# Optimization experiments

Hardware: AMD Instinct MI355X
Metric: run time of the kernel (lower is better)

The kernel has to match this reference:

```python
import jax, jax.numpy as jnp
import numpy as np

NEG = -9e15
ALPHA = 0.2  # leaky-relu slope


def gat_layer(h, mask, W, a, concat):
    # h: [N, Fin], W: [Fin, Fout], a: [2*Fout, 1], mask: [N, N]
    Wh = h @ W                                   # [N, Fout]
    F = Wh.shape[1]
    e = jax.nn.leaky_relu(Wh @ a[:F] + (Wh @ a[F:]).T, ALPHA)  # [N, N]
    att = jax.nn.softmax(jnp.where(mask > 0, e, NEG), axis=1)
    out = att @ Wh                               # [N, Fout]
    return jax.nn.elu(out) if concat else out


def gat(x, mask, W, a, Wo, ao):
    # W: [H, Fin, Fhid], a: [H, 2*Fhid, 1]
    heads = jax.vmap(lambda Wi, ai: gat_layer(x, mask, Wi, ai, True))(W, a)  # [H, N, Fhid]
    h = jnp.transpose(heads, (1, 0, 2)).reshape(x.shape[0], -1)  # [N, H*Fhid] (concat dim=1)
    return jax.nn.elu(gat_layer(h, mask, Wo, ao, False))


def setup_inputs() -> dict:
    key = jax.random.key(0)
    ks = jax.random.split(key, 16)
    N, Fin, H, Fhid, Ffin, P = 4096, 256, 4, 64, 64, 16
    x = jax.random.normal(ks[0], (N, Fin), jnp.float32)
    eye = jnp.eye(N, dtype=jnp.float32)
    sadj = jnp.maximum((jax.random.uniform(ks[1], (N, N)) < 0.005).astype(jnp.float32), eye)
    sadj2 = jnp.maximum((jax.random.uniform(ks[2], (N, N)) < 0.005).astype(jnp.float32), eye)
    s = 0.1
    inp = {
        "x": x, "sadj": sadj, "sadj2": sadj2,
        "W1": s * jax.random.normal(ks[3], (H, Fin, Fhid), jnp.float32),
        "a1": s * jax.random.normal(ks[4], (H, 2 * Fhid, 1), jnp.float32),
        "Wo1": s * jax.random.normal(ks[5], (H * Fhid, Ffin), jnp.float32),
        "ao1": s * jax.random.normal(ks[6], (2 * Ffin, 1), jnp.float32),
        "W2": s * jax.random.normal(ks[7], (H, Fin, Fhid), jnp.float32),
        "a2": s * jax.random.normal(ks[8], (H, 2 * Fhid, 1), jnp.float32),
        "Wo2": s * jax.random.normal(ks[9], (H * Fhid, Ffin), jnp.float32),
        "ao2": s * jax.random.normal(ks[10], (2 * Ffin, 1), jnp.float32),
        "Wp1": s * jax.random.normal(ks[11], (Ffin, P), jnp.float32),
        "bp1": jnp.zeros((P,), jnp.float32),
        "Wp2": s * jax.random.normal(ks[12], (P, 1), jnp.float32),
    }
    return inp


def reference(x, sadj, sadj2, W1, a1, Wo1, ao1, W2, a2, Wo2, ao2, Wp1, bp1, Wp2):
    emb1 = gat(x, sadj, W1, a1, Wo1, ao1)    # [N, Ffin]
    emb2 = gat(x, sadj2, W2, a2, Wo2, ao2)   # [N, Ffin]
    emb = jnp.stack([emb1, emb2], axis=1)    # [N, 2, Ffin]
    w = jnp.tanh(emb @ Wp1 + bp1) @ Wp2      # [N, 2, 1]
    beta = jax.nn.softmax(w, axis=1)
    return jnp.sum(beta * emb, axis=1)       # [N, Ffin]
```

## Files before the change

kernel.cpp:

```cpp
#include <hip/hip_runtime.h>
#include <hip/hip_bf16.h>
#include <stdint.h>


typedef short short8 __attribute__((ext_vector_type(8)));
typedef __bf16 bf16x8 __attribute__((ext_vector_type(8)));
typedef float floatx4 __attribute__((ext_vector_type(4)));

#define MAXDEG 128
#define LRELU 0.2f

template <typename V>
__device__ inline auto mfma_impl(V a, V b, floatx4 c, int)
    -> decltype(__builtin_amdgcn_mfma_f32_16x16x32_bf16(a, b, c, 0, 0, 0)) {
  return __builtin_amdgcn_mfma_f32_16x16x32_bf16(a, b, c, 0, 0, 0);
}
template <typename V>
__device__ inline floatx4 mfma_impl(V a, V b, floatx4 c, long) {
  return __builtin_amdgcn_mfma_f32_16x16x32_bf16(
      __builtin_bit_cast(bf16x8, a), __builtin_bit_cast(bf16x8, b), c, 0, 0, 0);
}
__device__ inline floatx4 MFMA16(short8 a, short8 b, floatx4 c) {
  return mfma_impl(a, b, c, 0);
}

__device__ inline bool is_bf16_inputs(const void* sadj) {
  return ((*(const uint32_t*)sadj) & 0xFFFFu) == 0x3F80u;
}
__device__ inline float ldval(const void* p, size_t i, bool isbf) {
  if (isbf) return __bfloat162float(((const __hip_bfloat16*)p)[i]);
  return ((const float*)p)[i];
}
__device__ inline uint16_t f2bf_bits(float f) {
  __hip_bfloat16 h = __float2bfloat16(f);
  return *(uint16_t*)&h;
}

static constexpr size_t OFF_ADJ = 0;
static constexpr size_t OFF_DEG = OFF_ADJ + (size_t)2 * 4096 * MAXDEG * 4;
static constexpr size_t OFF_XB  = OFF_DEG + (size_t)2 * 4096 * 4;
static constexpr size_t OFF_WT  = OFF_XB  + (size_t)4096 * 256 * 2;
static constexpr size_t OFF_WOT = OFF_WT  + (size_t)2 * 4 * 64 * 256 * 2;
static constexpr size_t OFF_AV  = OFF_WOT + (size_t)2 * 64 * 256 * 2;
static constexpr size_t OFF_AOV = OFF_AV  + (size_t)2 * 4 * 128 * 4;
static constexpr size_t OFF_WP1 = OFF_AOV + (size_t)2 * 128 * 4;
static constexpr size_t OFF_BP1 = OFF_WP1 + (size_t)64 * 16 * 4;
static constexpr size_t OFF_WP2 = OFF_BP1 + 64;
static constexpr size_t OFF_WH1 = OFF_WP2 + 192;
static constexpr size_t OFF_S1  = OFF_WH1 + (size_t)2 * 4096 * 256 * 4;
static constexpr size_t OFF_D1  = OFF_S1  + (size_t)2 * 4 * 4096 * 4;
static constexpr size_t OFF_H2  = OFF_D1  + (size_t)2 * 4 * 4096 * 4;
static constexpr size_t OFF_WH2 = OFF_H2  + (size_t)2 * 4096 * 256 * 2;
static constexpr size_t OFF_S2  = OFF_WH2 + (size_t)2 * 4096 * 64 * 4;
static constexpr size_t OFF_D2  = OFF_S2  + (size_t)2 * 4096 * 4;
static constexpr size_t OFF_EMB = OFF_D2  + (size_t)2 * 4096 * 4;

__global__ __launch_bounds__(256) void k_conv_x(const void* x, const void* sadj,
                                                uint16_t* xb) {
  bool isbf = is_bf16_inputs(sadj);
  int i0 = (blockIdx.x * 256 + threadIdx.x) * 4;
  if (isbf) {
    *(uint64_t*)(xb + i0) = *(const uint64_t*)((const uint16_t*)x + i0);
  } else {
    const float* xf = (const float*)x;
    float4 f = *(const float4*)(xf + i0);
    xb[i0 + 0] = f2bf_bits(f.x);
    xb[i0 + 1] = f2bf_bits(f.y);
    xb[i0 + 2] = f2bf_bits(f.z);
    xb[i0 + 3] = f2bf_bits(f.w);
  }
}

__global__ __launch_bounds__(256) void k_conv_w(const void* W1, const void* W2,
    const void* Wo1, const void* Wo2,
    const void* a1, const void* a2, const void* ao1, const void* ao2,
    const void* wp1, const void* bp1, const void* wp2, const void* sadj,
    uint16_t* Wt, uint16_t* Wot,
    float* Av, float* Aov, float* Wp1v, float* Bp1v, float* Wp2v) {
  bool isbf = is_bf16_inputs(sadj);
  int idx = blockIdx.x * 256 + threadIdx.x;
  if (idx < 131072) {
    int k = idx & 255, f = (idx >> 8) & 63, h = (idx >> 14) & 3, g = idx >> 16;
    const void* W = g ? W2 : W1;
    Wt[idx] = f2bf_bits(ldval(W, (size_t)h * 16384 + (size_t)k * 64 + f, isbf));
  } else if (idx < 163840) {
    int j = idx - 131072;
    int k = j & 255, f = (j >> 8) & 63, g = j >> 14;
    const void* W = g ? Wo2 : Wo1;
    Wot[j] = f2bf_bits(ldval(W, (size_t)k * 64 + f, isbf));
  } else if (idx < 166176) {
    int q = idx - 163840;
    if (q < 512)        Av[q] = ldval(a1, q, isbf);
    else if (q < 1024)  Av[q - 512 + 512] = 0.f, Av[q] = ldval(a2, q - 512, isbf);
    else if (q < 1152)  Aov[q - 1024] = ldval(ao1, q - 1024, isbf);
    else if (q < 1280)  Aov[q - 1152 + 128] = ldval(ao2, q - 1152, isbf);
    else if (q < 2304)  Wp1v[q - 1280] = ldval(wp1, q - 1280, isbf);
    else if (q < 2320)  Bp1v[q - 2304] = ldval(bp1, q - 2304, isbf);
    else                Wp2v[q - 2320] = ldval(wp2, q - 2320, isbf);
  }
}

__global__ __launch_bounds__(256) void k_adj(const void* sadj, const void* sadj2,
                                             int* adj, int* deg) {
  int w = blockIdx.x * 4 + (threadIdx.x >> 6);
  int lane = threadIdx.x & 63;
  int g = w >> 12, n = w & 4095;
  bool isbf = is_bf16_inputs(sadj);
  const void* mask = g ? sadj2 : sadj;
  int* out = adj + (size_t)w * MAXDEG;
  int cnt = 0;
  uint64_t ltmask = (1ull << lane) - 1ull;
  if (isbf) {
    const uint16_t* mrow = (const uint16_t*)mask + (size_t)n * 4096;
    for (int t = 0; t < 8; ++t) {
      int base = t * 512 + lane * 8;
      uint4 v = *(const uint4*)(mrow + base);
      uint32_t words[4] = {v.x, v.y, v.z, v.w};
#pragma unroll
      for (int k = 0; k < 8; ++k) {
        uint16_t val = (uint16_t)(words[k >> 1] >> ((k & 1) * 16));
        bool b = (val != 0) && !(val & 0x8000);
        uint64_t bal = __ballot(b);
        if (b) {
          int pos = cnt + __popcll(bal & ltmask);
          if (pos < MAXDEG) out[pos] = base + k;
        }
        cnt += __popcll(bal);
      }
    }
  } else {
    const float* mrow = (const float*)mask + (size_t)n * 4096;
    for (int t = 0; t < 16; ++t) {
      int base = t * 256 + lane * 4;
      float4 v = *(const float4*)(mrow + base);
      float vals[4] = {v.x, v.y, v.z, v.w};
#pragma unroll
      for (int k = 0; k < 4; ++k) {
        bool b = vals[k] > 0.f;
        uint64_t bal = __ballot(b);
        if (b) {
          int pos = cnt + __popcll(bal & ltmask);
          if (pos < MAXDEG) out[pos] = base + k;
        }
        cnt += __popcll(bal);
      }
    }
  }
  if (lane == 0) deg[w] = cnt < MAXDEG ? cnt : MAXDEG;
}

__global__ __launch_bounds__(256) void k_gemm1(const uint16_t* xb, const uint16_t* Wt,
                                               float* Wh1) {
  int w = blockIdx.x * 4 + (threadIdx.x >> 6);
  int lane = threadIdx.x & 63;
  int q = lane >> 4, c = lane & 15;
  int g = w >> 10, rem = w & 1023;
  int m0 = (rem >> 2) << 4, h = rem & 3;
  const uint16_t* B = Wt + (size_t)(g * 4 + h) * 64 * 256;
  floatx4 acc[4] = {};
  const uint16_t* arow = xb + (size_t)(m0 + c) * 256 + q * 8;
  for (int kk = 0; kk < 8; ++kk) {
    short8 a = *(const short8*)(arow + kk * 32);
#pragma unroll
    for (int t = 0; t < 4; ++t) {
      short8 b = *(const short8*)(B + (size_t)(t * 16 + c) * 256 + kk * 32 + q * 8);
      acc[t] = MFMA16(a, b, acc[t]);
    }
  }
  float* Crow = Wh1 + (size_t)(g * 4096 + m0) * 256 + h * 64;
#pragma unroll
  for (int t = 0; t < 4; ++t)
#pragma unroll
    for (int r = 0; r < 4; ++r)
      Crow[(size_t)(q * 4 + r) * 256 + t * 16 + c] = acc[t][r];
}

__global__ __launch_bounds__(256) void k_gemm2(const uint16_t* h2, const uint16_t* Wot,
                                               float* Wh2) {
  int w = blockIdx.x * 4 + (threadIdx.x >> 6);
  int lane = threadIdx.x & 63;
  int q = lane >> 4, c = lane & 15;
  int g = w >> 8, m0 = (w & 255) << 4;
  const uint16_t* A = h2 + (size_t)g * 4096 * 256;
  const uint16_t* B = Wot + (size_t)g * 64 * 256;
  floatx4 acc[4] = {};
  const uint16_t* arow = A + (size_t)(m0 + c) * 256 + q * 8;
  for (int kk = 0; kk < 8; ++kk) {
    short8 a = *(const short8*)(arow + kk * 32);
#pragma unroll
    for (int t = 0; t < 4; ++t) {
      short8 b = *(const short8*)(B + (size_t)(t * 16 + c) * 256 + kk * 32 + q * 8);
      acc[t] = MFMA16(a, b, acc[t]);
    }
  }
  float* Crow = Wh2 + (size_t)(g * 4096 + m0) * 64;
#pragma unroll
  for (int t = 0; t < 4; ++t)
#pragma unroll
    for (int r = 0; r < 4; ++r)
      Crow[(size_t)(q * 4 + r) * 64 + t * 16 + c] = acc[t][r];
}

__global__ __launch_bounds__(256) void k_sd1(const float* Wh1, const float* Av,
                                             float* s1, float* d1) {
  int w = blockIdx.x * 4 + (threadIdx.x >> 6);
  int lane = threadIdx.x & 63;
  int g = w >> 14, h = (w >> 12) & 3, n = w & 4095;
  float v = Wh1[((size_t)(g * 4096 + n)) * 256 + h * 64 + lane];
  const float* a = Av + (g * 4 + h) * 128;
  float ps = v * a[lane], pd = v * a[64 + lane];
#pragma unroll
  for (int o = 32; o; o >>= 1) {
    ps += __shfl_xor(ps, o);
    pd += __shfl_xor(pd, o);
  }
  if (lane == 0) {
    s1[((size_t)(g * 4096 + n)) * 4 + h] = ps;
    d1[((size_t)(g * 4096 + n)) * 4 + h] = pd;
  }
}

__global__ __launch_bounds__(256) void k_att1(const int* adj, const int* deg,
    const float* s1, const float* d1, const float* Wh1, uint16_t* h2) {
  __shared__ float pbuf[4][4][MAXDEG];
  __shared__ int jbuf[4][MAXDEG];
  int wv = threadIdx.x >> 6, lane = threadIdx.x & 63;
  int w = blockIdx.x * 4 + wv;
  int g = w >> 12;
  int gn = w;
  int dg = deg[gn];
  const int* nbr = adj + (size_t)gn * MAXDEG;
  float4 s4 = *(const float4*)(s1 + (size_t)gn * 4);
  const float4* d4 = (const float4*)(d1) + (size_t)g * 4096;

  bool v0 = lane < dg, v1 = lane + 64 < dg;
  int j0 = 0, j1 = 0;
  if (v0) j0 = nbr[lane];
  if (v1) j1 = nbr[lane + 64];
  float4 dj0 = d4[j0];
  float4 dj1 = d4[j1];
  if (v0) jbuf[wv][lane] = j0;
  if (v1) jbuf[wv][lane + 64] = j1;

  const float ninf = -3.0e38f;
  float sa[4] = {s4.x, s4.y, s4.z, s4.w};
  float d0a[4] = {dj0.x, dj0.y, dj0.z, dj0.w};
  float d1a[4] = {dj1.x, dj1.y, dj1.z, dj1.w};
#pragma unroll
  for (int h = 0; h < 4; ++h) {
    float t0 = sa[h] + d0a[h]; t0 = t0 > 0.f ? t0 : LRELU * t0;
    float t1 = sa[h] + d1a[h]; t1 = t1 > 0.f ? t1 : LRELU * t1;
    float e0 = v0 ? t0 : ninf;
    float e1 = v1 ? t1 : ninf;
    float m = fmaxf(e0, e1);
#pragma unroll
    for (int o = 32; o; o >>= 1) m = fmaxf(m, __shfl_xor(m, o));
    float p0 = v0 ? __expf(e0 - m) : 0.f;
    float p1 = v1 ? __expf(e1 - m) : 0.f;
    float l = p0 + p1;
#pragma unroll
    for (int o = 32; o; o >>= 1) l += __shfl_xor(l, o);
    float inv = __frcp_rn(l);
    pbuf[wv][h][lane] = p0 * inv;
    pbuf[wv][h][lane + 64] = p1 * inv;
  }
  int myh = lane >> 4;
  const float* prow = pbuf[wv][myh];
  const int* jb = jbuf[wv];
  const float4* Wg = (const float4*)(Wh1) + (size_t)g * 4096 * 64;
  float ax = 0.f, ay = 0.f, az = 0.f, aw = 0.f;
  int i = 0;
  for (; i + 4 <= dg; i += 4) {
    int ja = jb[i], jb2 = jb[i + 1], jc = jb[i + 2], jd = jb[i + 3];
    float pa = prow[i], pb = prow[i + 1], pc = prow[i + 2], pd = prow[i + 3];
    float4 wa = Wg[(size_t)ja * 64 + lane];
    float4 wb = Wg[(size_t)jb2 * 64 + lane];
    float4 wc = Wg[(size_t)jc * 64 + lane];
    float4 wd = Wg[(size_t)jd * 64 + lane];
    ax += pa * wa.x + pb * wb.x + pc * wc.x + pd * wd.x;
    ay += pa * wa.y + pb * wb.y + pc * wc.y + pd * wd.y;
    az += pa * wa.z + pb * wb.z + pc * wc.z + pd * wd.z;
    aw += pa * wa.w + pb * wb.w + pc * wc.w + pd * wd.w;
  }
  for (; i < dg; ++i) {
    int j = jb[i];
    float p = prow[i];
    float4 wa = Wg[(size_t)j * 64 + lane];
    ax += p * wa.x; ay += p * wa.y; az += p * wa.z; aw += p * wa.w;
  }
  ax = ax > 0.f ? ax : __expf(ax) - 1.f;
  ay = ay > 0.f ? ay : __expf(ay) - 1.f;
  az = az > 0.f ? az : __expf(az) - 1.f;
  aw = aw > 0.f ? aw : __expf(aw) - 1.f;
  ushort4 o4 = {f2bf_bits(ax), f2bf_bits(ay), f2bf_bits(az), f2bf_bits(aw)};
  *(ushort4*)(h2 + (size_t)gn * 256 + lane * 4) = o4;
}

__global__ __launch_bounds__(256) void k_sd2(const float* Wh2, const float* Aov,
                                             float* s2, float* d2) {
  int w = blockIdx.x * 4 + (threadIdx.x >> 6);
  int lane = threadIdx.x & 63;
  int g = w >> 12, n = w & 4095;
  float v = Wh2[((size_t)(g * 4096 + n)) * 64 + lane];
  const float* a = Aov + g * 128;
  float ps = v * a[lane], pd = v * a[64 + lane];
#pragma unroll
  for (int o = 32; o; o >>= 1) {
    ps += __shfl_xor(ps, o);
    pd += __shfl_xor(pd, o);
  }
  if (lane == 0) {
    s2[g * 4096 + n] = ps;
    d2[g * 4096 + n] = pd;
  }
}

__global__ __launch_bounds__(256) void k_att2(const int* adj, const int* deg,
    const float* s2, const float* d2, const float* Wh2, float* emb) {
  __shared__ float pbuf[4][MAXDEG];
  __shared__ int jbuf[4][MAXDEG];
  int wv = threadIdx.x >> 6, lane = threadIdx.x & 63;
  int w = blockIdx.x * 4 + wv;
  int g = w >> 12;
  int gn = w;
  int dg = deg[gn];
  const int* nbr = adj + (size_t)gn * MAXDEG;
  float sn = s2[gn];
  const float* dp = d2 + (size_t)g * 4096;

  bool v0 = lane < dg, v1 = lane + 64 < dg;
  int j0 = 0, j1 = 0;
  if (v0) j0 = nbr[lane];
  if (v1) j1 = nbr[lane + 64];
  float dd0 = dp[j0], dd1 = dp[j1];
  if (v0) jbuf[wv][lane] = j0;
  if (v1) jbuf[wv][lane + 64] = j1;

  const float ninf = -3.0e38f;
  float t0 = sn + dd0; t0 = t0 > 0.f ? t0 : LRELU * t0;
  float t1 = sn + dd1; t1 = t1 > 0.f ? t1 : LRELU * t1;
  float e0 = v0 ? t0 : ninf;
  float e1 = v1 ? t1 : ninf;
  float m = fmaxf(e0, e1);
#pragma unroll
  for (int o = 32; o; o >>= 1) m = fmaxf(m, __shfl_xor(m, o));
  float p0 = v0 ? __expf(e0 - m) : 0.f;
  float p1 = v1 ? __expf(e1 - m) : 0.f;
  float l = p0 + p1;
#pragma unroll
  for (int o = 32; o; o >>= 1) l += __shfl_xor(l, o);
  float inv = __frcp_rn(l);
  pbuf[wv][lane] = p0 * inv;
  pbuf[wv][lane + 64] = p1 * inv;

  int mye = lane >> 4, c4 = lane & 15;
  const float4* Wg = (const float4*)(Wh2) + (size_t)g * 4096 * 16;
  float ax = 0.f, ay = 0.f, az = 0.f, aw = 0.f;
  for (int i = 0; i < dg; i += 4) {
    int idx = i + mye;
    bool vv = idx < dg;
    int sidx = vv ? idx : 0;
    int j = jbuf[wv][sidx];
    float p = vv ? pbuf[wv][sidx] : 0.f;
    float4 wa = Wg[(size_t)j * 16 + c4];
    ax += p * wa.x; ay += p * wa.y; az += p * wa.z; aw += p * wa.w;
  }
#pragma unroll
  for (int o = 16; o <= 32; o <<= 1) {
    ax += __shfl_xor(ax, o);
    ay += __shfl_xor(ay, o);
    az += __shfl_xor(az, o);
    aw += __shfl_xor(aw, o);
  }
  if (lane < 16) {
    ax = ax > 0.f ? ax : __expf(ax) - 1.f;
    ay = ay > 0.f ? ay : __expf(ay) - 1.f;
    az = az > 0.f ? az : __expf(az) - 1.f;
    aw = aw > 0.f ? aw : __expf(aw) - 1.f;
    float4 r = {ax, ay, az, aw};
    *(float4*)(emb + (size_t)gn * 64 + lane * 4) = r;
  }
}

__global__ __launch_bounds__(256) void k_final(const float* emb, const float* Wp1v,
    const float* Bp1v, const float* Wp2v, const void* sadj, void* out) {
  __shared__ float se[4][128];
  __shared__ float st[4][32];
  __shared__ float sw[4][2];
  int wv = threadIdx.x >> 6, lane = threadIdx.x & 63;
  int n = blockIdx.x * 4 + wv;
  bool isbf = is_bf16_inputs(sadj);
  float e1 = emb[(size_t)n * 64 + lane];
  float e2 = emb[(size_t)(4096 + n) * 64 + lane];
  se[wv][lane] = e1;
  se[wv][64 + lane] = e2;
  __syncthreads();
  if (lane < 32) {
    int g = lane >> 4, p = lane & 15;
    float s = Bp1v[p];
    const float* eb = &se[wv][g * 64];
    for (int f = 0; f < 64; ++f) s += eb[f] * Wp1v[f * 16 + p];
    st[wv][lane] = tanhf(s);
  }
  __syncthreads();
  if (lane < 2) {
    float s = 0.f;
    for (int p = 0; p < 16; ++p) s += st[wv][lane * 16 + p] * Wp2v[p];
    sw[wv][lane] = s;
  }
  __syncthreads();
  float w0 = sw[wv][0], w1 = sw[wv][1];
  float mx = fmaxf(w0, w1);
  float p0 = __expf(w0 - mx), p1 = __expf(w1 - mx);
  float inv = 1.f / (p0 + p1);
  float v = (p0 * e1 + p1 * e2) * inv;
  if (isbf) ((uint16_t*)out)[(size_t)n * 64 + lane] = f2bf_bits(v);
  else ((float*)out)[(size_t)n * 64 + lane] = v;
}

extern "C" void kernel_launch(void* const* d_in, const int* in_sizes, int n_in,
                              void* d_out, int out_size, void* d_ws, size_t ws_size,
                              hipStream_t stream) {
  const void* x    = d_in[0];
  const void* sadj = d_in[1];
  const void* sadj2 = d_in[2];
  const void* W1  = d_in[3];
  const void* a1  = d_in[4];
  const void* Wo1 = d_in[5];
  const void* ao1 = d_in[6];
  const void* W2  = d_in[7];
  const void* a2  = d_in[8];
  const void* Wo2 = d_in[9];
  const void* ao2 = d_in[10];
  const void* Wp1 = d_in[11];
  const void* bp1 = d_in[12];
  const void* Wp2 = d_in[13];

  char* ws = (char*)d_ws;
  int* adj      = (int*)(ws + OFF_ADJ);
  int* deg      = (int*)(ws + OFF_DEG);
  uint16_t* xb  = (uint16_t*)(ws + OFF_XB);
  uint16_t* Wt  = (uint16_t*)(ws + OFF_WT);
  uint16_t* Wot = (uint16_t*)(ws + OFF_WOT);
  float* Av     = (float*)(ws + OFF_AV);
  float* Aov    = (float*)(ws + OFF_AOV);
  float* Wp1v   = (float*)(ws + OFF_WP1);
  float* Bp1v   = (float*)(ws + OFF_BP1);
  float* Wp2v   = (float*)(ws + OFF_WP2);
  float* Wh1    = (float*)(ws + OFF_WH1);
  float* s1     = (float*)(ws + OFF_S1);
  float* d1     = (float*)(ws + OFF_D1);
  uint16_t* h2  = (uint16_t*)(ws + OFF_H2);
  float* Wh2    = (float*)(ws + OFF_WH2);
  float* s2     = (float*)(ws + OFF_S2);
  float* d2     = (float*)(ws + OFF_D2);
  float* emb    = (float*)(ws + OFF_EMB);

  k_conv_x<<<1024, 256, 0, stream>>>(x, sadj, xb);
  k_conv_w<<<656, 256, 0, stream>>>(W1, W2, Wo1, Wo2, a1, a2, ao1, ao2,
                                    Wp1, bp1, Wp2, sadj,
                                    Wt, Wot, Av, Aov, Wp1v, Bp1v, Wp2v);
  k_adj<<<2048, 256, 0, stream>>>(sadj, sadj2, adj, deg);
  k_gemm1<<<512, 256, 0, stream>>>(xb, Wt, Wh1);
  k_sd1<<<8192, 256, 0, stream>>>(Wh1, Av, s1, d1);
  k_att1<<<2048, 256, 0, stream>>>(adj, deg, s1, d1, Wh1, h2);
  k_gemm2<<<128, 256, 0, stream>>>(h2, Wot, Wh2);
  k_sd2<<<2048, 256, 0, stream>>>(Wh2, Aov, s2, d2);
  k_att2<<<2048, 256, 0, stream>>>(adj, deg, s2, d2, Wh2, emb);
  k_final<<<1024, 256, 0, stream>>>(emb, Wp1v, Bp1v, Wp2v, sadj, d_out);
}
```

Before: 239.5 us.

## Fuse score projections into GEMMs, merge conversion kernels, rewrite adjacency compaction

Computes the per-node source/destination attention scores directly from the MFMA accumulators in both GEMM kernels, which removes the separate sd1/sd2 kernels and their re-reads of Wh. It merges the x and weight conversion kernels into one launch. The adjacency builder now issues all row loads up front, builds a per-lane bitmask, and uses a wave prefix scan to place neighbours, replacing one ballot per element. Neighbour order becomes lane-major rather than column-sorted, and each lane writes scattered indices.

```diff
diff --git a/kernel.cpp b/kernel.cpp
--- a/kernel.cpp
+++ b/kernel.cpp
@@ -55,30 +55,29 @@
 static constexpr size_t OFF_D2  = OFF_S2  + (size_t)2 * 4096 * 4;
 static constexpr size_t OFF_EMB = OFF_D2  + (size_t)2 * 4096 * 4;
 
-__global__ __launch_bounds__(256) void k_conv_x(const void* x, const void* sadj,
-                                                uint16_t* xb) {
-  bool isbf = is_bf16_inputs(sadj);
-  int i0 = (blockIdx.x * 256 + threadIdx.x) * 4;
-  if (isbf) {
-    *(uint64_t*)(xb + i0) = *(const uint64_t*)((const uint16_t*)x + i0);
-  } else {
-    const float* xf = (const float*)x;
-    float4 f = *(const float4*)(xf + i0);
-    xb[i0 + 0] = f2bf_bits(f.x);
-    xb[i0 + 1] = f2bf_bits(f.y);
-    xb[i0 + 2] = f2bf_bits(f.z);
-    xb[i0 + 3] = f2bf_bits(f.w);
-  }
-}
-
-__global__ __launch_bounds__(256) void k_conv_w(const void* W1, const void* W2,
-    const void* Wo1, const void* Wo2,
+__global__ __launch_bounds__(256) void k_conv(const void* x,
+    const void* W1, const void* W2, const void* Wo1, const void* Wo2,
     const void* a1, const void* a2, const void* ao1, const void* ao2,
     const void* wp1, const void* bp1, const void* wp2, const void* sadj,
-    uint16_t* Wt, uint16_t* Wot,
+    uint16_t* xb, uint16_t* Wt, uint16_t* Wot,
     float* Av, float* Aov, float* Wp1v, float* Bp1v, float* Wp2v) {
   bool isbf = is_bf16_inputs(sadj);
-  int idx = blockIdx.x * 256 + threadIdx.x;
+  int bid = blockIdx.x;
+  if (bid < 1024) {
+    int i0 = (bid * 256 + threadIdx.x) * 4;
+    if (isbf) {
+      *(uint64_t*)(xb + i0) = *(const uint64_t*)((const uint16_t*)x + i0);
+    } else {
+      const float* xf = (const float*)x;
+      float4 f = *(const float4*)(xf + i0);
+      xb[i0 + 0] = f2bf_bits(f.x);
+      xb[i0 + 1] = f2bf_bits(f.y);
+      xb[i0 + 2] = f2bf_bits(f.z);
+      xb[i0 + 3] = f2bf_bits(f.w);
+    }
+    return;
+  }
+  int idx = (bid - 1024) * 256 + threadIdx.x;
   if (idx < 131072) {
     int k = idx & 255, f = (idx >> 8) & 63, h = (idx >> 14) & 3, g = idx >> 16;
     const void* W = g ? W2 : W1;
@@ -91,7 +90,7 @@
   } else if (idx < 166176) {
     int q = idx - 163840;
     if (q < 512)        Av[q] = ldval(a1, q, isbf);
-    else if (q < 1024)  Av[q - 512 + 512] = 0.f, Av[q] = ldval(a2, q - 512, isbf);
+    else if (q < 1024)  Av[q] = ldval(a2, q - 512, isbf);
     else if (q < 1152)  Aov[q - 1024] = ldval(ao1, q - 1024, isbf);
     else if (q < 1280)  Aov[q - 1152 + 128] = ldval(ao2, q - 1152, isbf);
     else if (q < 2304)  Wp1v[q - 1280] = ldval(wp1, q - 1280, isbf);
@@ -108,49 +107,57 @@
   bool isbf = is_bf16_inputs(sadj);
   const void* mask = g ? sadj2 : sadj;
   int* out = adj + (size_t)w * MAXDEG;
-  int cnt = 0;
-  uint64_t ltmask = (1ull << lane) - 1ull;
+  uint64_t bits = 0;
   if (isbf) {
     const uint16_t* mrow = (const uint16_t*)mask + (size_t)n * 4096;
+    uint4 v[8];
+#pragma unroll
+    for (int t = 0; t < 8; ++t) v[t] = *(const uint4*)(mrow + t * 512 + lane * 8);
+#pragma unroll
     for (int t = 0; t < 8; ++t) {
-      int base = t * 512 + lane * 8;
-      uint4 v = *(const uint4*)(mrow + base);
-      uint32_t words[4] = {v.x, v.y, v.z, v.w};
+      uint32_t wd[4] = {v[t].x, v[t].y, v[t].z, v[t].w};
 #pragma unroll
       for (int k = 0; k < 8; ++k) {
-        uint16_t val = (uint16_t)(words[k >> 1] >> ((k & 1) * 16));
-        bool b = (val != 0) && !(val & 0x8000);
-        uint64_t bal = __ballot(b);
-        if (b) {
-          int pos = cnt + __popcll(bal & ltmask);
-          if (pos < MAXDEG) out[pos] = base + k;
-        }
-        cnt += __popcll(bal);
+        uint16_t val = (uint16_t)(wd[k >> 1] >> ((k & 1) * 16));
+        if (val != 0 && !(val & 0x8000)) bits |= 1ull << (t * 8 + k);
       }
     }
   } else {
     const float* mrow = (const float*)mask + (size_t)n * 4096;
+    float4 v[16];
+#pragma unroll
+    for (int t = 0; t < 16; ++t) v[t] = *(const float4*)(mrow + t * 256 + lane * 4);
+#pragma unroll
     for (int t = 0; t < 16; ++t) {
-      int base = t * 256 + lane * 4;
-      float4 v = *(const float4*)(mrow + base);
-      float vals[4] = {v.x, v.y, v.z, v.w};
-#pragma unroll
-      for (int k = 0; k < 4; ++k) {
-        bool b = vals[k] > 0.f;
-        uint64_t bal = __ballot(b);
-        if (b) {
-          int pos = cnt + __popcll(bal & ltmask);
-          if (pos < MAXDEG) out[pos] = base + k;
-        }
-        cnt += __popcll(bal);
-      }
-    }
-  }
-  if (lane == 0) deg[w] = cnt < MAXDEG ? cnt : MAXDEG;
+      float vals[4] = {v[t].x, v[t].y, v[t].z, v[t].w};
+#pragma unroll
+      for (int k = 0; k < 4; ++k)
+        if (vals[k] > 0.f) bits |= 1ull << (t * 4 + k);
+    }
+  }
+  int c = __popcll(bits);
+  int pre = c;
+#pragma unroll
+  for (int o = 1; o < 64; o <<= 1) {
+    int tv = __shfl_up(pre, o);
+    if (lane >= o) pre += tv;
+  }
+  int total = __shfl(pre, 63);
+  int off = pre - c;
+  while (bits) {
+    int i = __ffsll((unsigned long long)bits) - 1;
+    bits &= bits - 1;
+    int col = isbf ? ((i >> 3) * 512 + lane * 8 + (i & 7))
+                   : ((i >> 2) * 256 + lane * 4 + (i & 3));
+    if (off < MAXDEG) out[off] = col;
+    ++off;
+  }
+  if (lane == 0) deg[w] = total < MAXDEG ? total : MAXDEG;
 }
 
 __global__ __launch_bounds__(256) void k_gemm1(const uint16_t* xb, const uint16_t* Wt,
-                                               float* Wh1) {
+                                               const float* Av,
+                                               float* Wh1, float* s1, float* d1) {
   int w = blockIdx.x * 4 + (threadIdx.x >> 6);
   int lane = threadIdx.x & 63;
   int q = lane >> 4, c = lane & 15;
@@ -173,10 +180,28 @@
 #pragma unroll
     for (int r = 0; r < 4; ++r)
       Crow[(size_t)(q * 4 + r) * 256 + t * 16 + c] = acc[t][r];
+  const float* ag = Av + (g * 4 + h) * 128;
+  float as[4], ad[4];
+#pragma unroll
+  for (int t = 0; t < 4; ++t) { as[t] = ag[t * 16 + c]; ad[t] = ag[64 + t * 16 + c]; }
+#pragma unroll
+  for (int r = 0; r < 4; ++r) {
+    float ps = 0.f, pd = 0.f;
+#pragma unroll
+    for (int t = 0; t < 4; ++t) { ps += acc[t][r] * as[t]; pd += acc[t][r] * ad[t]; }
+#pragma unroll
+    for (int o = 1; o < 16; o <<= 1) { ps += __shfl_xor(ps, o); pd += __shfl_xor(pd, o); }
+    if (c == 0) {
+      int n = m0 + q * 4 + r;
+      s1[((size_t)(g * 4096 + n)) * 4 + h] = ps;
+      d1[((size_t)(g * 4096 + n)) * 4 + h] = pd;
+    }
+  }
 }
 
 __global__ __launch_bounds__(256) void k_gemm2(const uint16_t* h2, const uint16_t* Wot,
-                                               float* Wh2) {
+                                               const float* Aov,
+                                               float* Wh2, float* s2, float* d2) {
   int w = blockIdx.x * 4 + (threadIdx.x >> 6);
   int lane = threadIdx.x & 63;
   int q = lane >> 4, c = lane & 15;
@@ -199,24 +224,22 @@
 #pragma unroll
     for (int r = 0; r < 4; ++r)
       Crow[(size_t)(q * 4 + r) * 64 + t * 16 + c] = acc[t][r];
-}
-
-__global__ __launch_bounds__(256) void k_sd1(const float* Wh1, const float* Av,
-                                             float* s1, float* d1) {
-  int w = blockIdx.x * 4 + (threadIdx.x >> 6);
-  int lane = threadIdx.x & 63;
-  int g = w >> 14, h = (w >> 12) & 3, n = w & 4095;
-  float v = Wh1[((size_t)(g * 4096 + n)) * 256 + h * 64 + lane];
-  const float* a = Av + (g * 4 + h) * 128;
-  float ps = v * a[lane], pd = v * a[64 + lane];
-#pragma unroll
-  for (int o = 32; o; o >>= 1) {
-    ps += __shfl_xor(ps, o);
-    pd += __shfl_xor(pd, o);
-  }
-  if (lane == 0) {
-    s1[((size_t)(g * 4096 + n)) * 4 + h] = ps;
-    d1[((size_t)(g * 4096 + n)) * 4 + h] = pd;
+  const float* ag = Aov + g * 128;
+  float as[4], ad[4];
+#pragma unroll
+  for (int t = 0; t < 4; ++t) { as[t] = ag[t * 16 + c]; ad[t] = ag[64 + t * 16 + c]; }
+#pragma unroll
+  for (int r = 0; r < 4; ++r) {
+    float ps = 0.f, pd = 0.f;
+#pragma unroll
+    for (int t = 0; t < 4; ++t) { ps += acc[t][r] * as[t]; pd += acc[t][r] * ad[t]; }
+#pragma unroll
+    for (int o = 1; o < 16; o <<= 1) { ps += __shfl_xor(ps, o); pd += __shfl_xor(pd, o); }
+    if (c == 0) {
+      int n = m0 + q * 4 + r;
+      s2[g * 4096 + n] = ps;
+      d2[g * 4096 + n] = pd;
+    }
   }
 }
 
@@ -294,25 +317,6 @@
   aw = aw > 0.f ? aw : __expf(aw) - 1.f;
   ushort4 o4 = {f2bf_bits(ax), f2bf_bits(ay), f2bf_bits(az), f2bf_bits(aw)};
   *(ushort4*)(h2 + (size_t)gn * 256 + lane * 4) = o4;
-}
-
-__global__ __launch_bounds__(256) void k_sd2(const float* Wh2, const float* Aov,
-                                             float* s2, float* d2) {
-  int w = blockIdx.x * 4 + (threadIdx.x >> 6);
-  int lane = threadIdx.x & 63;
-  int g = w >> 12, n = w & 4095;
-  float v = Wh2[((size_t)(g * 4096 + n)) * 64 + lane];
-  const float* a = Aov + g * 128;
-  float ps = v * a[lane], pd = v * a[64 + lane];
-#pragma unroll
-  for (int o = 32; o; o >>= 1) {
-    ps += __shfl_xor(ps, o);
-    pd += __shfl_xor(pd, o);
-  }
-  if (lane == 0) {
-    s2[g * 4096 + n] = ps;
-    d2[g * 4096 + n] = pd;
-  }
 }
 
 __global__ __launch_bounds__(256) void k_att2(const int* adj, const int* deg,
@@ -456,16 +460,13 @@
   float* d2     = (float*)(ws + OFF_D2);
   float* emb    = (float*)(ws + OFF_EMB);
 
-  k_conv_x<<<1024, 256, 0, stream>>>(x, sadj, xb);
-  k_conv_w<<<656, 256, 0, stream>>>(W1, W2, Wo1, Wo2, a1, a2, ao1, ao2,
-                                    Wp1, bp1, Wp2, sadj,
-                                    Wt, Wot, Av, Aov, Wp1v, Bp1v, Wp2v);
+  k_conv<<<1680, 256, 0, stream>>>(x, W1, W2, Wo1, Wo2, a1, a2, ao1, ao2,
+                                   Wp1, bp1, Wp2, sadj,
+                                   xb, Wt, Wot, Av, Aov, Wp1v, Bp1v, Wp2v);
   k_adj<<<2048, 256, 0, stream>>>(sadj, sadj2, adj, deg);
-  k_gemm1<<<512, 256, 0, stream>>>(xb, Wt, Wh1);
-  k_sd1<<<8192, 256, 0, stream>>>(Wh1, Av, s1, d1);
+  k_gemm1<<<512, 256, 0, stream>>>(xb, Wt, Av, Wh1, s1, d1);
   k_att1<<<2048, 256, 0, stream>>>(adj, deg, s1, d1, Wh1, h2);
-  k_gemm2<<<128, 256, 0, stream>>>(h2, Wot, Wh2);
-  k_sd2<<<2048, 256, 0, stream>>>(Wh2, Aov, s2, d2);
+  k_gemm2<<<128, 256, 0, stream>>>(h2, Wot, Aov, Wh2, s2, d2);
   k_att2<<<2048, 256, 0, stream>>>(adj, deg, s2, d2, Wh2, emb);
   k_final<<<1024, 256, 0, stream>>>(emb, Wp1v, Bp1v, Wp2v, sadj, d_out);
 }
```

Result: faster. 229.5 us (-4.2%).
